# Kernel tuning notes

Measured on AMD Instinct MI355X. Metric: run time of the kernel, lower is better.

Reference implementation:

```python
import jax, jax.numpy as jnp
import numpy as np

N_CLASSES = 9
INPUT_SIZE = N_CLASSES + 1  # 10
HIDDEN = 512
BATCH = 256
SEQ = 1024


def setup_inputs() -> dict:
    key = jax.random.key(0)
    ks = jax.random.split(key, 7)
    s_ih = 1.0 / np.sqrt(HIDDEN)
    inputs = jax.random.normal(ks[0], (BATCH, SEQ, INPUT_SIZE), dtype=jnp.float32)
    # LSTMCell params (PyTorch layout: [4H, in], gate order i,f,g,o)
    W_ih = jax.random.uniform(ks[1], (4 * HIDDEN, INPUT_SIZE), jnp.float32, -s_ih, s_ih)
    W_hh = jax.random.uniform(ks[2], (4 * HIDDEN, HIDDEN), jnp.float32, -s_ih, s_ih)
    b_ih = jax.random.uniform(ks[3], (4 * HIDDEN,), jnp.float32, -s_ih, s_ih)
    b_hh = jax.random.uniform(ks[4], (4 * HIDDEN,), jnp.float32, -s_ih, s_ih)
    # Output projection: kaiming_normal_ (fan_in = HIDDEN, relu gain sqrt(2)), zero bias
    lin_W = jax.random.normal(ks[5], (N_CLASSES, HIDDEN), dtype=jnp.float32) * np.float32(np.sqrt(2.0 / HIDDEN))
    lin_b = jnp.zeros((N_CLASSES,), dtype=jnp.float32)
    return {"inputs": inputs, "W_ih": W_ih, "W_hh": W_hh, "b_ih": b_ih,
            "b_hh": b_hh, "lin_W": lin_W, "lin_b": lin_b}


def reference(inputs, W_ih, W_hh, b_ih, b_hh, lin_W, lin_b):
    B = inputs.shape[0]
    H = W_hh.shape[1]
    # Precompute input contributions for all steps in one big GEMM: [B,T,4H]
    x_gates = jnp.einsum('bti,gi->btg', inputs, W_ih) + b_ih + b_hh

    def step(carry, xg_t):
        h, c = carry
        gates = xg_t + h @ W_hh.T  # [B, 4H]
        i, f, g, o = jnp.split(gates, 4, axis=-1)
        i = jax.nn.sigmoid(i)
        f = jax.nn.sigmoid(f)
        g = jnp.tanh(g)
        o = jax.nn.sigmoid(o)
        c = f * c + i * g
        h = o * jnp.tanh(c)
        return (h, c), h

    h0 = jnp.zeros((B, H), dtype=inputs.dtype)
    c0 = jnp.zeros((B, H), dtype=inputs.dtype)
    _, hs = jax.lax.scan(step, (h0, c0), jnp.swapaxes(x_gates, 0, 1))  # hs: [T,B,H]
    # Per-step Linear, batched into one GEMM: [B,T,n_classes]
    logits = jnp.einsum('tbh,ch->btc', hs, lin_W) + lin_b
    return logits
```

## Files before the change

kernel.cpp:

```cpp
#include <hip/hip_runtime.h>

typedef unsigned int u32;
typedef unsigned long long u64;
typedef unsigned short u16;
typedef short bfrag __attribute__((ext_vector_type(8)));
typedef float f4 __attribute__((ext_vector_type(4)));
typedef u32 u32x4 __attribute__((ext_vector_type(4)));

#define HID 512
#define SEQT 1024
#define NIN 10
#define NC 9
#define NCL 16
#define MB  16
#define KSN 17
#define HROW 512
#define LROW 516

#define WPACK_U16 (16*4*2*KSN*64*8)
#define WPACK_BYTES (WPACK_U16*2)
#define HEX_U16 (NCL*2*MB*HROW)
#define HEX_BYTES (HEX_U16*2)
#define FLAGS_U32 (NCL*64)
#define FLAGS_BYTES (FLAGS_U32*4)

__device__ __forceinline__ u16 f2b(float f){
  u32 u = __float_as_uint(f);
  return (u16)((u + 0x7fffu + ((u>>16)&1u)) >> 16);
}
__device__ __forceinline__ float b2f(u16 b){ return __uint_as_float(((u32)b)<<16); }
__device__ __forceinline__ float sigm(float x){ return 1.f/(1.f+__expf(-x)); }
__device__ __forceinline__ float tanh_(float x){ float e=__expf(2.f*x); return 1.f - 2.f/(e+1.f); }

__device__ __forceinline__ void st32_sys(u64 base, u32 off, u32 v){
  asm volatile("global_store_dword %0, %1, %2 sc0 sc1" :: "v"(off), "v"(v), "s"(base) : "memory");
}
__device__ __forceinline__ void st128_sys(u64 base, u32 off, u32x4 v){
  asm volatile("global_store_dwordx4 %0, %1, %2 sc0 sc1" :: "v"(off), "v"(v), "s"(base) : "memory");
}
__device__ __forceinline__ void drain_vm(){
  asm volatile("s_waitcnt vmcnt(0)" ::: "memory");
}
__device__ __forceinline__ void spin_flags(u64 flgb, u32 foff, u32 tgt){
  u32 v0, v1 = 0;
  asm volatile("global_load_dword %0, %1, %2 sc0 sc1" : "=&v"(v0) : "v"(foff), "s"(flgb) : "memory");
  int guard = 0;
  for(;;){
    asm volatile("global_load_dword %0, %1, %2 sc0 sc1\n\ts_waitcnt vmcnt(1)"
                 : "=&v"(v1) : "v"(foff), "s"(flgb) : "memory");
    if (__all((int)(v0 >= tgt))) break;
    asm volatile("global_load_dword %0, %1, %2 sc0 sc1\n\ts_waitcnt vmcnt(1)"
                 : "=&v"(v0) : "v"(foff), "s"(flgb) : "memory");
    if (__all((int)(v1 >= tgt))) break;
    if ((guard += 2) > 400000) break;
  }
  drain_vm();
  asm volatile("" :: "v"(v0), "v"(v1));
}

__global__ void pack_kernel(const float* __restrict__ W_ih, const float* __restrict__ W_hh,
                            const float* __restrict__ b_ih, const float* __restrict__ b_hh,
                            u16* __restrict__ Wpack)
{
  int tid = blockIdx.x*256 + threadIdx.x;
  if (tid >= 16*4*2*KSN*64) return;
  int lane = tid & 63;
  int rest = tid >> 6;
  int ks = rest % KSN; rest /= KSN;
  int p = rest & 1; rest >>= 1;
  int w = rest & 3; rest >>= 2;
  int g = rest;
  int c2 = lane & 15;
  int kb = lane >> 4;
  int j = g*32 + w*8 + (c2 & 7);
  int gate = (p ? 2 : 0) + (c2 >= 8 ? 1 : 0);
  int R = gate*HID + j;

  union { u16 s[8]; bfrag v; } o;
  if (ks < 16) {
    const float* src = W_hh + (size_t)R*HID + ks*32 + kb*8;
    #pragma unroll
    for (int e=0;e<8;e++) o.s[e] = f2b(src[e]);
  } else {
    #pragma unroll
    for (int e=0;e<8;e++) {
      int k = kb*8 + e;
      float v = (k < NIN) ? W_ih[(size_t)R*NIN + k] : (k==NIN ? (b_ih[R]+b_hh[R]) : 0.f);
      o.s[e] = f2b(v);
    }
  }
  *(bfrag*)(Wpack + (size_t)tid*8) = o.v;
}

__global__ void init_kernel(u16* __restrict__ hex_, u32* __restrict__ flags)
{
  int tid = blockIdx.x*256 + threadIdx.x;
  if (tid < HEX_U16) hex_[tid] = 0;
  if (tid < FLAGS_U32) flags[tid] = 0;
}

__global__ __launch_bounds__(256, 1) void lstm_kernel(
    const float* __restrict__ inputs, const float* __restrict__ lin_W,
    const float* __restrict__ lin_b, const u16* __restrict__ Wpack,
    u16* __restrict__ hex_, u32* __restrict__ flags, float* __restrict__ out)
{
  const int bid = blockIdx.x;
  const int cl = bid >> 4;
  const int g = bid & 15;
  const int tid = threadIdx.x;
  const int w = tid >> 6;
  const int lane = tid & 63;
  const int c2 = lane & 15;
  const int kb = lane >> 4;
  const int jb = g*32 + w*8;
  const bool lowhalf = (c2 < 8);
  const int vb = cl*MB + g;

  __shared__ __align__(16) u16 panel[MB*LROW];
  __shared__ __align__(16) u16 rowbuf[2][HID];

  bfrag wf0[KSN], wf1[KSN];
  {
    const u16* base = Wpack + ((size_t)(g*4+w)*2)*KSN*64*8;
    #pragma unroll
    for (int ks=0;ks<KSN;ks++) wf0[ks] = *(const bfrag*)(base + ((size_t)ks*64 + lane)*8);
    #pragma unroll
    for (int ks=0;ks<KSN;ks++) wf1[ks] = *(const bfrag*)(base + ((size_t)(KSN+ks)*64 + lane)*8);
  }
  float lw[3][8]; float lb[3];
  if (w < 3) {
    #pragma unroll
    for (int cc=0;cc<3;cc++){
      int cls = w*3+cc;
      lb[cc] = lin_b[cls];
      #pragma unroll
      for (int e=0;e<8;e++) lw[cc][e] = lin_W[(size_t)cls*HID + lane*8 + e];
    }
  }

  float cst[4] = {0.f,0.f,0.f,0.f};

  const u64 ex0 = (u64)(hex_ + (size_t)(cl*2+0)*MB*HROW);
  const u64 ex1 = (u64)(hex_ + (size_t)(cl*2+1)*MB*HROW);
  const u64 flgb = (u64)(flags + (size_t)cl*64);
  const u32 foff = (u32)(lane*4);

  u32 go[4], lo[4];
  #pragma unroll
  for (int i=0;i<4;i++){
    u32 chunk = (u32)tid + (u32)i*256u;
    go[i] = (chunk>>6)*1024u + (chunk&63u)*16u;
    lo[i] = (chunk>>6)*(LROW*2u) + (chunk&63u)*16u;
  }

  const float* xrow = inputs + (size_t)(cl*MB + c2)*SEQT*NIN;

  for (int t = 0; t < SEQT; ++t) {
    const u64 cur = (t & 1) ? ex1 : ex0;
    const u64 nxt = (t & 1) ? ex0 : ex1;

    union { u32 u[4]; bfrag v; } xu;
    xu.u[0]=0; xu.u[1]=0; xu.u[2]=0; xu.u[3]=0;
    {
      const float* p = xrow + (size_t)t*NIN;
      if (kb == 0) {
        #pragma unroll
        for (int q=0;q<4;q++) xu.u[q] = (u32)f2b(p[2*q]) | ((u32)f2b(p[2*q+1])<<16);
      } else if (kb == 1) {
        xu.u[0] = (u32)f2b(p[8]) | ((u32)f2b(p[9])<<16);
        xu.u[1] = 0x3F80u;
      }
    }

    if (w == 0) spin_flags(flgb, foff, (u32)t);
    __syncthreads();

    u32x4 r0,r1,r2,r3;
    asm volatile(
      "global_load_dwordx4 %0, %4, %8 sc0 sc1\n\t"
      "global_load_dwordx4 %1, %5, %8 sc0 sc1\n\t"
      "global_load_dwordx4 %2, %6, %8 sc0 sc1\n\t"
      "global_load_dwordx4 %3, %7, %8 sc0 sc1"
      : "=&v"(r0), "=&v"(r1), "=&v"(r2), "=&v"(r3)
      : "v"(go[0]), "v"(go[1]), "v"(go[2]), "v"(go[3]), "s"(cur)
      : "memory");

    if (w < 3 && t >= 2) {
      bfrag hx = *(const bfrag*)&rowbuf[(t-1)&1][lane*8];
      float hv[8];
      #pragma unroll
      for (int e=0;e<8;e++) hv[e] = b2f((u16)hx[e]);
      #pragma unroll
      for (int cc=0;cc<3;cc++){
        float s = 0.f;
        #pragma unroll
        for (int e=0;e<8;e++) s += hv[e]*lw[cc][e];
        #pragma unroll
        for (int off=1;off<64;off<<=1) s += __shfl_xor(s, off, 64);
        if (lane == 0)
          out[((size_t)vb*SEQT + (t-2))*NC + (w*3+cc)] = s + lb[cc];
      }
    }

    drain_vm();
    __builtin_amdgcn_sched_barrier(0);
    *(u32x4*)((char*)panel + lo[0]) = r0;
    *(u32x4*)((char*)panel + lo[1]) = r1;
    *(u32x4*)((char*)panel + lo[2]) = r2;
    *(u32x4*)((char*)panel + lo[3]) = r3;
    __syncthreads();

    if (w == 3)
      *(bfrag*)&rowbuf[t&1][lane*8] = *(const bfrag*)&panel[g*LROW + lane*8];

    f4 acc0 = {0.f,0.f,0.f,0.f}, acc1 = {0.f,0.f,0.f,0.f};
    #pragma unroll
    for (int ks=0;ks<16;ks++){
      bfrag av = *(const bfrag*)&panel[c2*LROW + ks*32 + kb*8];
      acc0 = __builtin_amdgcn_mfma_f32_16x16x32_bf16(av, wf0[ks], acc0, 0,0,0);
      acc1 = __builtin_amdgcn_mfma_f32_16x16x32_bf16(av, wf1[ks], acc1, 0,0,0);
    }
    acc0 = __builtin_amdgcn_mfma_f32_16x16x32_bf16(xu.v, wf0[16], acc0, 0,0,0);
    acc1 = __builtin_amdgcn_mfma_f32_16x16x32_bf16(xu.v, wf1[16], acc1, 0,0,0);

    u16 hb[4];
    #pragma unroll
    for (int r=0;r<4;r++){
      float a0 = sigm(acc0[r]);
      float a1 = lowhalf ? tanh_(acc1[r]) : sigm(acc1[r]);
      float p0 = __shfl_xor(a0, 8, 64);
      float p1 = __shfl_xor(a1, 8, 64);
      float ii = lowhalf ? a0 : p0;
      float ff = lowhalf ? p0 : a0;
      float gg = lowhalf ? a1 : p1;
      float oo = lowhalf ? p1 : a1;
      float cn = ff*cst[r] + ii*gg;
      cst[r] = cn;
      hb[r] = f2b(oo * tanh_(cn));
    }

    #pragma unroll
    for (int r=0;r<4;r++){
      u32 pv = (u32)hb[r] | (((u32)(u16)__shfl_down((int)hb[r], 1, 64)) << 16);
      u32 p1 = __shfl_down(pv, 2, 64);
      u32 p2 = __shfl_down(pv, 4, 64);
      u32 p3 = __shfl_down(pv, 6, 64);
      if (c2 == 0) {
        u32x4 pk = {pv, p1, p2, p3};
        st128_sys(nxt, (u32)((kb*4+r)*1024 + jb*2), pk);
      }
    }

    drain_vm();
    if (lane == 0)
      st32_sys(flgb, (u32)((g*4+w)*4), (u32)(t+1));
  }

  if (w == 0) spin_flags(flgb, foff, (u32)SEQT);
  __syncthreads();
  if (w < 3) {
    {
      bfrag hx = *(const bfrag*)&rowbuf[(SEQT-1)&1][lane*8];
      float hv[8];
      #pragma unroll
      for (int e=0;e<8;e++) hv[e] = b2f((u16)hx[e]);
      #pragma unroll
      for (int cc=0;cc<3;cc++){
        float s = 0.f;
        #pragma unroll
        for (int e=0;e<8;e++) s += hv[e]*lw[cc][e];
        #pragma unroll
        for (int off=1;off<64;off<<=1) s += __shfl_xor(s, off, 64);
        if (lane == 0)
          out[((size_t)vb*SEQT + (SEQT-2))*NC + (w*3+cc)] = s + lb[cc];
      }
    }
    {
      u32x4 rr;
      asm volatile("global_load_dwordx4 %0, %1, %2 sc0 sc1\n\ts_waitcnt vmcnt(0)"
                   : "=&v"(rr) : "v"((u32)(g*1024 + lane*16)), "s"(ex0) : "memory");
      float hv[8];
      #pragma unroll
      for (int e=0;e<4;e++){
        hv[2*e]   = b2f((u16)(rr[e] & 0xffffu));
        hv[2*e+1] = b2f((u16)(rr[e] >> 16));
      }
      #pragma unroll
      for (int cc=0;cc<3;cc++){
        float s = 0.f;
        #pragma unroll
        for (int e=0;e<8;e++) s += hv[e]*lw[cc][e];
        #pragma unroll
        for (int off=1;off<64;off<<=1) s += __shfl_xor(s, off, 64);
        if (lane == 0)
          out[((size_t)vb*SEQT + (SEQT-1))*NC + (w*3+cc)] = s + lb[cc];
      }
    }
  }
}

extern "C" void kernel_launch(void* const* d_in, const int* in_sizes, int n_in,
                              void* d_out, int out_size, void* d_ws, size_t ws_size,
                              hipStream_t stream)
{
  const float* inputs = (const float*)d_in[0];
  const float* W_ih   = (const float*)d_in[1];
  const float* W_hh   = (const float*)d_in[2];
  const float* b_ih   = (const float*)d_in[3];
  const float* b_hh   = (const float*)d_in[4];
  const float* lin_W  = (const float*)d_in[5];
  const float* lin_b  = (const float*)d_in[6];

  u16* Wpack = (u16*)d_ws;
  u16* hex_  = (u16*)((char*)d_ws + WPACK_BYTES);
  u32* flags = (u32*)((char*)d_ws + WPACK_BYTES + HEX_BYTES);

  pack_kernel<<<(16*4*2*KSN*64 + 255)/256, 256, 0, stream>>>(W_ih, W_hh, b_ih, b_hh, Wpack);
  init_kernel<<<(HEX_U16 + 255)/256, 256, 0, stream>>>(hex_, flags);
  lstm_kernel<<<256, 256, 0, stream>>>(inputs, lin_W, lin_b, Wpack, hex_, flags, (float*)d_out);
}
```

Before: 4.223 ms.

## Replace flag-based barrier with per-word tagged hidden-state exchange polling

Each bf16 hidden value is now stored with the timestep tag in the low 16 bits of a 32-bit word. Consumers poll the data itself until every tag matches, instead of waiting on separate per-wave flags and then reloading the data. This removes the store-drain, flag-store, flag-spin and second-load round trip on every step. The block's own slice is written straight into a double-buffered LDS panel, and the output projection reads the panel directly. In exchange the exchange traffic doubles in size, and the polling loads are repeated for any chunks not yet ready.

Measured after the change: 5.087 ms. 1.2x slower.

```diff
diff --git a/kernel.cpp b/kernel.cpp
--- a/kernel.cpp
+++ b/kernel.cpp
@@ -6,6 +6,7 @@
 typedef short bfrag __attribute__((ext_vector_type(8)));
 typedef float f4 __attribute__((ext_vector_type(4)));
 typedef u32 u32x4 __attribute__((ext_vector_type(4)));
+typedef u32 u32x2 __attribute__((ext_vector_type(2)));
 
 #define HID 512
 #define SEQT 1024
@@ -14,15 +15,12 @@
 #define NCL 16
 #define MB  16
 #define KSN 17
-#define HROW 512
 #define LROW 516
 
 #define WPACK_U16 (16*4*2*KSN*64*8)
 #define WPACK_BYTES (WPACK_U16*2)
-#define HEX_U16 (NCL*2*MB*HROW)
-#define HEX_BYTES (HEX_U16*2)
-#define FLAGS_U32 (NCL*64)
-#define FLAGS_BYTES (FLAGS_U32*4)
+#define HEX_U32 (NCL*2*MB*HID)
+#define HEX_BYTES (HEX_U32*4)
 
 __device__ __forceinline__ u16 f2b(float f){
   u32 u = __float_as_uint(f);
@@ -34,28 +32,6 @@
 
 __device__ __forceinline__ void st32_sys(u64 base, u32 off, u32 v){
   asm volatile("global_store_dword %0, %1, %2 sc0 sc1" :: "v"(off), "v"(v), "s"(base) : "memory");
-}
-__device__ __forceinline__ void st128_sys(u64 base, u32 off, u32x4 v){
-  asm volatile("global_store_dwordx4 %0, %1, %2 sc0 sc1" :: "v"(off), "v"(v), "s"(base) : "memory");
-}
-__device__ __forceinline__ void drain_vm(){
-  asm volatile("s_waitcnt vmcnt(0)" ::: "memory");
-}
-__device__ __forceinline__ void spin_flags(u64 flgb, u32 foff, u32 tgt){
-  u32 v0, v1 = 0;
-  asm volatile("global_load_dword %0, %1, %2 sc0 sc1" : "=&v"(v0) : "v"(foff), "s"(flgb) : "memory");
-  int guard = 0;
-  for(;;){
-    asm volatile("global_load_dword %0, %1, %2 sc0 sc1\n\ts_waitcnt vmcnt(1)"
-                 : "=&v"(v1) : "v"(foff), "s"(flgb) : "memory");
-    if (__all((int)(v0 >= tgt))) break;
-    asm volatile("global_load_dword %0, %1, %2 sc0 sc1\n\ts_waitcnt vmcnt(1)"
-                 : "=&v"(v0) : "v"(foff), "s"(flgb) : "memory");
-    if (__all((int)(v1 >= tgt))) break;
-    if ((guard += 2) > 400000) break;
-  }
-  drain_vm();
-  asm volatile("" :: "v"(v0), "v"(v1));
 }
 
 __global__ void pack_kernel(const float* __restrict__ W_ih, const float* __restrict__ W_hh,
@@ -92,17 +68,27 @@
   *(bfrag*)(Wpack + (size_t)tid*8) = o.v;
 }
 
-__global__ void init_kernel(u16* __restrict__ hex_, u32* __restrict__ flags)
+__global__ void init_kernel(u32* __restrict__ hexw)
 {
   int tid = blockIdx.x*256 + threadIdx.x;
-  if (tid < HEX_U16) hex_[tid] = 0;
-  if (tid < FLAGS_U32) flags[tid] = 0;
-}
+  if (tid < HEX_U32) hexw[tid] = 0;
+}
+
+#define PISS(i, vi) \
+  if (pend & (1u<<(i))) { \
+    asm volatile("global_load_dwordx4 %0, %1, %2 sc0 sc1" \
+                 : "=&v"(vi) : "v"(gof[i]), "s"(cur) : "memory"); }
+#define PCHK(i, vi) \
+  if (pend & (1u<<(i))) { \
+    if ((((vi[0]^tg)|(vi[1]^tg)|(vi[2]^tg)|(vi[3]^tg)) & 0xffffu) == 0u) { \
+      u32x2 pk = { (vi[0]>>16) | (vi[1]&0xffff0000u), (vi[2]>>16) | (vi[3]&0xffff0000u) }; \
+      *(u32x2*)((char*)panb + lof[i]) = pk; \
+      pend &= ~(1u<<(i)); } }
 
 __global__ __launch_bounds__(256, 1) void lstm_kernel(
     const float* __restrict__ inputs, const float* __restrict__ lin_W,
     const float* __restrict__ lin_b, const u16* __restrict__ Wpack,
-    u16* __restrict__ hex_, u32* __restrict__ flags, float* __restrict__ out)
+    u32* __restrict__ hexw, float* __restrict__ out)
 {
   const int bid = blockIdx.x;
   const int cl = bid >> 4;
@@ -116,8 +102,7 @@
   const bool lowhalf = (c2 < 8);
   const int vb = cl*MB + g;
 
-  __shared__ __align__(16) u16 panel[MB*LROW];
-  __shared__ __align__(16) u16 rowbuf[2][HID];
+  __shared__ __align__(16) u16 panel[2][MB*LROW];
 
   bfrag wf0[KSN], wf1[KSN];
   {
@@ -140,24 +125,29 @@
 
   float cst[4] = {0.f,0.f,0.f,0.f};
 
-  const u64 ex0 = (u64)(hex_ + (size_t)(cl*2+0)*MB*HROW);
-  const u64 ex1 = (u64)(hex_ + (size_t)(cl*2+1)*MB*HROW);
-  const u64 flgb = (u64)(flags + (size_t)cl*64);
-  const u32 foff = (u32)(lane*4);
-
-  u32 go[4], lo[4];
+  const u64 ex0 = (u64)(hexw + (size_t)(cl*2+0)*MB*HID);
+  const u64 ex1 = (u64)(hexw + (size_t)(cl*2+1)*MB*HID);
+
+  u32 gof[8], lof[8], pend0 = 0;
   #pragma unroll
-  for (int i=0;i<4;i++){
-    u32 chunk = (u32)tid + (u32)i*256u;
-    go[i] = (chunk>>6)*1024u + (chunk&63u)*16u;
-    lo[i] = (chunk>>6)*(LROW*2u) + (chunk&63u)*16u;
-  }
+  for (int i=0;i<8;i++){
+    u32 c = (u32)tid + (u32)i*256u;
+    u32 row = c >> 7, rem = c & 127u;
+    gof[i] = row*2048u + rem*16u;
+    lof[i] = row*(LROW*2u) + rem*8u;
+    if ((int)(rem >> 3) != g) pend0 |= (1u<<i);
+  }
+
+  for (int i = tid; i < MB*LROW; i += 256) panel[0][i] = 0;
 
   const float* xrow = inputs + (size_t)(cl*MB + c2)*SEQT*NIN;
 
   for (int t = 0; t < SEQT; ++t) {
     const u64 cur = (t & 1) ? ex1 : ex0;
     const u64 nxt = (t & 1) ? ex0 : ex1;
+    const u32 tg  = (u32)t;
+    const u32 tgn = (u32)(t+1);
+    u16* panb = &panel[t&1][0];
 
     union { u32 u[4]; bfrag v; } xu;
     xu.u[0]=0; xu.u[1]=0; xu.u[2]=0; xu.u[3]=0;
@@ -172,51 +162,27 @@
       }
     }
 
-    if (w == 0) spin_flags(flgb, foff, (u32)t);
+    {
+      u32 pend = pend0;
+      u32x4 v0,v1,v2,v3,v4,v5,v6,v7;
+      for (int gq = 0; pend && gq < 20000; ++gq) {
+        PISS(0,v0) PISS(1,v1) PISS(2,v2) PISS(3,v3)
+        PISS(4,v4) PISS(5,v5) PISS(6,v6) PISS(7,v7)
+        asm volatile("s_waitcnt vmcnt(0)" ::: "memory");
+        __builtin_amdgcn_sched_barrier(0);
+        PCHK(0,v0) PCHK(1,v1) PCHK(2,v2) PCHK(3,v3)
+        PCHK(4,v4) PCHK(5,v5) PCHK(6,v6) PCHK(7,v7)
+      }
+    }
     __syncthreads();
 
-    u32x4 r0,r1,r2,r3;
-    asm volatile(
-      "global_load_dwordx4 %0, %4, %8 sc0 sc1\n\t"
-      "global_load_dwordx4 %1, %5, %8 sc0 sc1\n\t"
-      "global_load_dwordx4 %2, %6, %8 sc0 sc1\n\t"
-      "global_load_dwordx4 %3, %7, %8 sc0 sc1"
-      : "=&v"(r0), "=&v"(r1), "=&v"(r2), "=&v"(r3)
-      : "v"(go[0]), "v"(go[1]), "v"(go[2]), "v"(go[3]), "s"(cur)
-      : "memory");
-
-    if (w < 3 && t >= 2) {
-      bfrag hx = *(const bfrag*)&rowbuf[(t-1)&1][lane*8];
-      float hv[8];
-      #pragma unroll
-      for (int e=0;e<8;e++) hv[e] = b2f((u16)hx[e]);
-      #pragma unroll
-      for (int cc=0;cc<3;cc++){
-        float s = 0.f;
-        #pragma unroll
-        for (int e=0;e<8;e++) s += hv[e]*lw[cc][e];
-        #pragma unroll
-        for (int off=1;off<64;off<<=1) s += __shfl_xor(s, off, 64);
-        if (lane == 0)
-          out[((size_t)vb*SEQT + (t-2))*NC + (w*3+cc)] = s + lb[cc];
-      }
-    }
-
-    drain_vm();
-    __builtin_amdgcn_sched_barrier(0);
-    *(u32x4*)((char*)panel + lo[0]) = r0;
-    *(u32x4*)((char*)panel + lo[1]) = r1;
-    *(u32x4*)((char*)panel + lo[2]) = r2;
-    *(u32x4*)((char*)panel + lo[3]) = r3;
-    __syncthreads();
-
-    if (w == 3)
-      *(bfrag*)&rowbuf[t&1][lane*8] = *(const bfrag*)&panel[g*LROW + lane*8];
+    bfrag hx;
+    if (w < 3) hx = *(const bfrag*)&panb[g*LROW + lane*8];
 
     f4 acc0 = {0.f,0.f,0.f,0.f}, acc1 = {0.f,0.f,0.f,0.f};
     #pragma unroll
     for (int ks=0;ks<16;ks++){
-      bfrag av = *(const bfrag*)&panel[c2*LROW + ks*32 + kb*8];
+      bfrag av = *(const bfrag*)&panb[c2*LROW + ks*32 + kb*8];
       acc0 = __builtin_amdgcn_mfma_f32_16x16x32_bf16(av, wf0[ks], acc0, 0,0,0);
       acc1 = __builtin_amdgcn_mfma_f32_16x16x32_bf16(av, wf1[ks], acc1, 0,0,0);
     }
@@ -239,28 +205,20 @@
       hb[r] = f2b(oo * tanh_(cn));
     }
 
-    #pragma unroll
-    for (int r=0;r<4;r++){
-      u32 pv = (u32)hb[r] | (((u32)(u16)__shfl_down((int)hb[r], 1, 64)) << 16);
-      u32 p1 = __shfl_down(pv, 2, 64);
-      u32 p2 = __shfl_down(pv, 4, 64);
-      u32 p3 = __shfl_down(pv, 6, 64);
-      if (c2 == 0) {
-        u32x4 pk = {pv, p1, p2, p3};
-        st128_sys(nxt, (u32)((kb*4+r)*1024 + jb*2), pk);
-      }
-    }
-
-    drain_vm();
-    if (lane == 0)
-      st32_sys(flgb, (u32)((g*4+w)*4), (u32)(t+1));
-  }
-
-  if (w == 0) spin_flags(flgb, foff, (u32)SEQT);
-  __syncthreads();
-  if (w < 3) {
     {
-      bfrag hx = *(const bfrag*)&rowbuf[(SEQT-1)&1][lane*8];
+      int col = jb + (c2 & 7);
+      u32 rowa = (u32)(kb*4 + (lowhalf ? 0 : 2));
+      u16 slo = lowhalf ? hb[0] : hb[2];
+      u16 shi = lowhalf ? hb[1] : hb[3];
+      u32 cb4 = (u32)(col*4);
+      st32_sys(nxt, rowa*2048u + cb4,        ((u32)slo<<16) | tgn);
+      st32_sys(nxt, rowa*2048u + 2048u + cb4, ((u32)shi<<16) | tgn);
+      u16* pn = &panel[(t+1)&1][0];
+      pn[rowa*LROW + col]     = slo;
+      pn[(rowa+1)*LROW + col] = shi;
+    }
+
+    if (w < 3 && t > 0) {
       float hv[8];
       #pragma unroll
       for (int e=0;e<8;e++) hv[e] = b2f((u16)hx[e]);
@@ -272,29 +230,44 @@
         #pragma unroll
         for (int off=1;off<64;off<<=1) s += __shfl_xor(s, off, 64);
         if (lane == 0)
-          out[((size_t)vb*SEQT + (SEQT-2))*NC + (w*3+cc)] = s + lb[cc];
+          out[((size_t)vb*SEQT + (t-1))*NC + (w*3+cc)] = s + lb[cc];
       }
     }
-    {
-      u32x4 rr;
-      asm volatile("global_load_dwordx4 %0, %1, %2 sc0 sc1\n\ts_waitcnt vmcnt(0)"
-                   : "=&v"(rr) : "v"((u32)(g*1024 + lane*16)), "s"(ex0) : "memory");
-      float hv[8];
-      #pragma unroll
-      for (int e=0;e<4;e++){
-        hv[2*e]   = b2f((u16)(rr[e] & 0xffffu));
-        hv[2*e+1] = b2f((u16)(rr[e] >> 16));
-      }
-      #pragma unroll
-      for (int cc=0;cc<3;cc++){
-        float s = 0.f;
-        #pragma unroll
-        for (int e=0;e<8;e++) s += hv[e]*lw[cc][e];
-        #pragma unroll
-        for (int off=1;off<64;off<<=1) s += __shfl_xor(s, off, 64);
-        if (lane == 0)
-          out[((size_t)vb*SEQT + (SEQT-1))*NC + (w*3+cc)] = s + lb[cc];
-      }
+  }
+
+  if (w < 3) {
+    u32 ge0 = (u32)(g*2048 + (lane*2)*16);
+    u32 ge1 = ge0 + 16u;
+    u32x4 e0, e1;
+    u32 pend = 3u;
+    const u32 tg = (u32)SEQT;
+    for (int gq = 0; pend && gq < 20000; ++gq) {
+      if (pend & 1u)
+        asm volatile("global_load_dwordx4 %0, %1, %2 sc0 sc1"
+                     : "=&v"(e0) : "v"(ge0), "s"(ex0) : "memory");
+      if (pend & 2u)
+        asm volatile("global_load_dwordx4 %0, %1, %2 sc0 sc1"
+                     : "=&v"(e1) : "v"(ge1), "s"(ex0) : "memory");
+      asm volatile("s_waitcnt vmcnt(0)" ::: "memory");
+      __builtin_amdgcn_sched_barrier(0);
+      if ((pend & 1u) && ((((e0[0]^tg)|(e0[1]^tg)|(e0[2]^tg)|(e0[3]^tg)) & 0xffffu)==0u)) pend &= ~1u;
+      if ((pend & 2u) && ((((e1[0]^tg)|(e1[1]^tg)|(e1[2]^tg)|(e1[3]^tg)) & 0xffffu)==0u)) pend &= ~2u;
+    }
+    float hv[8];
+    #pragma unroll
+    for (int e=0;e<4;e++){
+      hv[e]   = __uint_as_float(e0[e] & 0xffff0000u);
+      hv[4+e] = __uint_as_float(e1[e] & 0xffff0000u);
+    }
+    #pragma unroll
+    for (int cc=0;cc<3;cc++){
+      float s = 0.f;
+      #pragma unroll
+      for (int e=0;e<8;e++) s += hv[e]*lw[cc][e];
+      #pragma unroll
+      for (int off=1;off<64;off<<=1) s += __shfl_xor(s, off, 64);
+      if (lane == 0)
+        out[((size_t)vb*SEQT + (SEQT-1))*NC + (w*3+cc)] = s + lb[cc];
     }
   }
 }
@@ -312,10 +285,9 @@
   const float* lin_b  = (const float*)d_in[6];
 
   u16* Wpack = (u16*)d_ws;
-  u16* hex_  = (u16*)((char*)d_ws + WPACK_BYTES);
-  u32* flags = (u32*)((char*)d_ws + WPACK_BYTES + HEX_BYTES);
+  u32* hexw  = (u32*)((char*)d_ws + WPACK_BYTES);
 
   pack_kernel<<<(16*4*2*KSN*64 + 255)/256, 256, 0, stream>>>(W_ih, W_hh, b_ih, b_hh, Wpack);
-  init_kernel<<<(HEX_U16 + 255)/256, 256, 0, stream>>>(hex_, flags);
-  lstm_kernel<<<256, 256, 0, stream>>>(inputs, lin_W, lin_b, Wpack, hex_, flags, (float*)d_out);
-}
+  init_kernel<<<(HEX_U32 + 255)/256, 256, 0, stream>>>(hexw);
+  lstm_kernel<<<256, 256, 0, stream>>>(inputs, lin_W, lin_b, Wpack, hexw, (float*)d_out);
+}
```

## Interleave two batch groups per block to overlap cross-block sync latency

Applied to the files above, without the earlier changes.

Each block now processes two independent 16-row batch groups in alternation, so one group's flag wait and exchange can overlap the other group's compute. The grid is halved to 128 blocks, and each block uses 16 per-block flags instead of per-wave flags, with a __syncthreads before the flag store. The h exchange layout becomes contiguous and uses 32-bit stores, and the output projection reads h directly from the panel. The cost is serialized per-group work inside each block and extra barriers; with only 8 clusters, latency may still dominate.

Result: slower. 9.623 ms (+127.9%).

```diff
diff --git a/kernel.cpp b/kernel.cpp
--- a/kernel.cpp
+++ b/kernel.cpp
@@ -11,17 +11,18 @@
 #define SEQT 1024
 #define NIN 10
 #define NC 9
-#define NCL 16
-#define MB  16
+#define NCLS 8
+#define NG 2
+#define MB 16
 #define KSN 17
-#define HROW 512
 #define LROW 516
 
 #define WPACK_U16 (16*4*2*KSN*64*8)
 #define WPACK_BYTES (WPACK_U16*2)
-#define HEX_U16 (NCL*2*MB*HROW)
+#define PANEL_BYTES (MB*HID*2)
+#define HEX_U16 (NCLS*NG*2*MB*HID)
 #define HEX_BYTES (HEX_U16*2)
-#define FLAGS_U32 (NCL*64)
+#define FLAGS_U32 (NCLS*NG*64)
 #define FLAGS_BYTES (FLAGS_U32*4)
 
 __device__ __forceinline__ u16 f2b(float f){
@@ -35,27 +36,18 @@
 __device__ __forceinline__ void st32_sys(u64 base, u32 off, u32 v){
   asm volatile("global_store_dword %0, %1, %2 sc0 sc1" :: "v"(off), "v"(v), "s"(base) : "memory");
 }
-__device__ __forceinline__ void st128_sys(u64 base, u32 off, u32x4 v){
-  asm volatile("global_store_dwordx4 %0, %1, %2 sc0 sc1" :: "v"(off), "v"(v), "s"(base) : "memory");
-}
 __device__ __forceinline__ void drain_vm(){
   asm volatile("s_waitcnt vmcnt(0)" ::: "memory");
 }
 __device__ __forceinline__ void spin_flags(u64 flgb, u32 foff, u32 tgt){
-  u32 v0, v1 = 0;
-  asm volatile("global_load_dword %0, %1, %2 sc0 sc1" : "=&v"(v0) : "v"(foff), "s"(flgb) : "memory");
   int guard = 0;
   for(;;){
-    asm volatile("global_load_dword %0, %1, %2 sc0 sc1\n\ts_waitcnt vmcnt(1)"
-                 : "=&v"(v1) : "v"(foff), "s"(flgb) : "memory");
-    if (__all((int)(v0 >= tgt))) break;
-    asm volatile("global_load_dword %0, %1, %2 sc0 sc1\n\ts_waitcnt vmcnt(1)"
-                 : "=&v"(v0) : "v"(foff), "s"(flgb) : "memory");
-    if (__all((int)(v1 >= tgt))) break;
-    if ((guard += 2) > 400000) break;
-  }
-  drain_vm();
-  asm volatile("" :: "v"(v0), "v"(v1));
+    u32 v;
+    asm volatile("global_load_dword %0, %1, %2 sc0 sc1\n\ts_waitcnt vmcnt(0)"
+                 : "=&v"(v) : "v"(foff), "s"(flgb) : "memory");
+    if (__all((int)(v >= tgt))) break;
+    if (++guard > 200000) break;
+  }
 }
 
 __global__ void pack_kernel(const float* __restrict__ W_ih, const float* __restrict__ W_hh,
@@ -114,10 +106,8 @@
   const int kb = lane >> 4;
   const int jb = g*32 + w*8;
   const bool lowhalf = (c2 < 8);
-  const int vb = cl*MB + g;
-
-  __shared__ __align__(16) u16 panel[MB*LROW];
-  __shared__ __align__(16) u16 rowbuf[2][HID];
+
+  __shared__ __align__(16) u16 panel[NG][MB*LROW];
 
   bfrag wf0[KSN], wf1[KSN];
   {
@@ -138,58 +128,143 @@
     }
   }
 
-  float cst[4] = {0.f,0.f,0.f,0.f};
-
-  const u64 ex0 = (u64)(hex_ + (size_t)(cl*2+0)*MB*HROW);
-  const u64 ex1 = (u64)(hex_ + (size_t)(cl*2+1)*MB*HROW);
-  const u64 flgb = (u64)(flags + (size_t)cl*64);
-  const u32 foff = (u32)(lane*4);
+  float cst[NG][4] = {{0.f,0.f,0.f,0.f},{0.f,0.f,0.f,0.f}};
+
+  u64 exp0[NG], exp1[NG], flgb[NG];
+  const float* xrow[NG];
+  int vb[NG];
+  #pragma unroll
+  for (int grp=0; grp<NG; ++grp){
+    exp0[grp] = (u64)((char*)hex_ + (size_t)((cl*NG+grp)*2+0)*PANEL_BYTES);
+    exp1[grp] = (u64)((char*)hex_ + (size_t)((cl*NG+grp)*2+1)*PANEL_BYTES);
+    flgb[grp] = (u64)(flags + (size_t)(cl*NG+grp)*64);
+    xrow[grp] = inputs + (size_t)(cl*32 + grp*16 + c2)*SEQT*NIN;
+    vb[grp]   = cl*32 + grp*16 + g;
+  }
+  const u32 foff = (u32)(c2*4);
 
   u32 go[4], lo[4];
   #pragma unroll
   for (int i=0;i<4;i++){
     u32 chunk = (u32)tid + (u32)i*256u;
-    go[i] = (chunk>>6)*1024u + (chunk&63u)*16u;
+    go[i] = chunk*16u;
     lo[i] = (chunk>>6)*(LROW*2u) + (chunk&63u)*16u;
   }
 
-  const float* xrow = inputs + (size_t)(cl*MB + c2)*SEQT*NIN;
-
   for (int t = 0; t < SEQT; ++t) {
-    const u64 cur = (t & 1) ? ex1 : ex0;
-    const u64 nxt = (t & 1) ? ex0 : ex1;
-
-    union { u32 u[4]; bfrag v; } xu;
-    xu.u[0]=0; xu.u[1]=0; xu.u[2]=0; xu.u[3]=0;
-    {
-      const float* p = xrow + (size_t)t*NIN;
-      if (kb == 0) {
+    #pragma unroll
+    for (int grp=0; grp<NG; ++grp) {
+      const u64 cur = (t & 1) ? exp1[grp] : exp0[grp];
+      const u64 nxt = (t & 1) ? exp0[grp] : exp1[grp];
+      u16* panb = &panel[grp][0];
+
+      spin_flags(flgb[grp], foff, (u32)t);
+
+      u32x4 r0,r1,r2,r3;
+      asm volatile(
+        "global_load_dwordx4 %0, %4, %8 sc0 sc1\n\t"
+        "global_load_dwordx4 %1, %5, %8 sc0 sc1\n\t"
+        "global_load_dwordx4 %2, %6, %8 sc0 sc1\n\t"
+        "global_load_dwordx4 %3, %7, %8 sc0 sc1"
+        : "=&v"(r0), "=&v"(r1), "=&v"(r2), "=&v"(r3)
+        : "v"(go[0]), "v"(go[1]), "v"(go[2]), "v"(go[3]), "s"(cur)
+        : "memory");
+
+      union { u32 u[4]; bfrag v; } xu;
+      xu.u[0]=0; xu.u[1]=0; xu.u[2]=0; xu.u[3]=0;
+      {
+        const float* p = xrow[grp] + (size_t)t*NIN;
+        if (kb == 0) {
+          #pragma unroll
+          for (int q=0;q<4;q++) xu.u[q] = (u32)f2b(p[2*q]) | ((u32)f2b(p[2*q+1])<<16);
+        } else if (kb == 1) {
+          xu.u[0] = (u32)f2b(p[8]) | ((u32)f2b(p[9])<<16);
+          xu.u[1] = 0x3F80u;
+        }
+      }
+
+      drain_vm();
+      __builtin_amdgcn_sched_barrier(0);
+      *(u32x4*)((char*)panb + lo[0]) = r0;
+      *(u32x4*)((char*)panb + lo[1]) = r1;
+      *(u32x4*)((char*)panb + lo[2]) = r2;
+      *(u32x4*)((char*)panb + lo[3]) = r3;
+      __syncthreads();
+
+      bfrag hx;
+      if (w < 3) hx = *(const bfrag*)&panb[g*LROW + lane*8];
+
+      f4 acc0 = {0.f,0.f,0.f,0.f}, acc1 = {0.f,0.f,0.f,0.f};
+      #pragma unroll
+      for (int ks=0;ks<16;ks++){
+        bfrag av = *(const bfrag*)&panb[c2*LROW + ks*32 + kb*8];
+        acc0 = __builtin_amdgcn_mfma_f32_16x16x32_bf16(av, wf0[ks], acc0, 0,0,0);
+        acc1 = __builtin_amdgcn_mfma_f32_16x16x32_bf16(av, wf1[ks], acc1, 0,0,0);
+      }
+      acc0 = __builtin_amdgcn_mfma_f32_16x16x32_bf16(xu.v, wf0[16], acc0, 0,0,0);
+      acc1 = __builtin_amdgcn_mfma_f32_16x16x32_bf16(xu.v, wf1[16], acc1, 0,0,0);
+
+      u16 hb[4];
+      #pragma unroll
+      for (int r=0;r<4;r++){
+        float a0 = sigm(acc0[r]);
+        float a1 = lowhalf ? tanh_(acc1[r]) : sigm(acc1[r]);
+        float p0 = __shfl_xor(a0, 8, 64);
+        float p1 = __shfl_xor(a1, 8, 64);
+        float ii = lowhalf ? a0 : p0;
+        float ff = lowhalf ? p0 : a0;
+        float gg = lowhalf ? a1 : p1;
+        float oo = lowhalf ? p1 : a1;
+        float cn = ff*cst[grp][r] + ii*gg;
+        cst[grp][r] = cn;
+        hb[r] = f2b(oo * tanh_(cn));
+      }
+
+      #pragma unroll
+      for (int r=0;r<4;r++){
+        u32 nb = (u32)(u16)__shfl_down((int)hb[r], 1, 64);
+        if (lowhalf && !(c2 & 1)) {
+          u32 pv = (u32)hb[r] | (nb << 16);
+          st32_sys(nxt, (u32)((kb*4+r)*1024 + (jb + c2)*2), pv);
+        }
+      }
+
+      drain_vm();
+      __syncthreads();
+      if (tid == 0)
+        st32_sys(flgb[grp], (u32)(g*4), (u32)(t+1));
+
+      if (w < 3 && t > 0) {
+        float hv[8];
         #pragma unroll
-        for (int q=0;q<4;q++) xu.u[q] = (u32)f2b(p[2*q]) | ((u32)f2b(p[2*q+1])<<16);
-      } else if (kb == 1) {
-        xu.u[0] = (u32)f2b(p[8]) | ((u32)f2b(p[9])<<16);
-        xu.u[1] = 0x3F80u;
+        for (int e=0;e<8;e++) hv[e] = b2f((u16)hx[e]);
+        #pragma unroll
+        for (int cc=0;cc<3;cc++){
+          float s = 0.f;
+          #pragma unroll
+          for (int e=0;e<8;e++) s += hv[e]*lw[cc][e];
+          #pragma unroll
+          for (int off=1;off<64;off<<=1) s += __shfl_xor(s, off, 64);
+          if (lane == 0)
+            out[((size_t)vb[grp]*SEQT + (t-1))*NC + (w*3+cc)] = s + lb[cc];
+        }
       }
     }
-
-    if (w == 0) spin_flags(flgb, foff, (u32)t);
-    __syncthreads();
-
-    u32x4 r0,r1,r2,r3;
-    asm volatile(
-      "global_load_dwordx4 %0, %4, %8 sc0 sc1\n\t"
-      "global_load_dwordx4 %1, %5, %8 sc0 sc1\n\t"
-      "global_load_dwordx4 %2, %6, %8 sc0 sc1\n\t"
-      "global_load_dwordx4 %3, %7, %8 sc0 sc1"
-      : "=&v"(r0), "=&v"(r1), "=&v"(r2), "=&v"(r3)
-      : "v"(go[0]), "v"(go[1]), "v"(go[2]), "v"(go[3]), "s"(cur)
-      : "memory");
-
-    if (w < 3 && t >= 2) {
-      bfrag hx = *(const bfrag*)&rowbuf[(t-1)&1][lane*8];
+  }
+
+  #pragma unroll
+  for (int grp=0; grp<NG; ++grp) {
+    spin_flags(flgb[grp], foff, (u32)SEQT);
+    if (w < 3) {
+      u32x4 rr;
+      asm volatile("global_load_dwordx4 %0, %1, %2 sc0 sc1\n\ts_waitcnt vmcnt(0)"
+                   : "=&v"(rr) : "v"((u32)(g*1024 + lane*16)), "s"(exp0[grp]) : "memory");
       float hv[8];
       #pragma unroll
-      for (int e=0;e<8;e++) hv[e] = b2f((u16)hx[e]);
+      for (int e=0;e<4;e++){
+        hv[2*e]   = b2f((u16)(rr[e] & 0xffffu));
+        hv[2*e+1] = b2f((u16)(rr[e] >> 16));
+      }
       #pragma unroll
       for (int cc=0;cc<3;cc++){
         float s = 0.f;
@@ -198,102 +273,7 @@
         #pragma unroll
         for (int off=1;off<64;off<<=1) s += __shfl_xor(s, off, 64);
         if (lane == 0)
-          out[((size_t)vb*SEQT + (t-2))*NC + (w*3+cc)] = s + lb[cc];
-      }
-    }
-
-    drain_vm();
-    __builtin_amdgcn_sched_barrier(0);
-    *(u32x4*)((char*)panel + lo[0]) = r0;
-    *(u32x4*)((char*)panel + lo[1]) = r1;
-    *(u32x4*)((char*)panel + lo[2]) = r2;
-    *(u32x4*)((char*)panel + lo[3]) = r3;
-    __syncthreads();
-
-    if (w == 3)
-      *(bfrag*)&rowbuf[t&1][lane*8] = *(const bfrag*)&panel[g*LROW + lane*8];
-
-    f4 acc0 = {0.f,0.f,0.f,0.f}, acc1 = {0.f,0.f,0.f,0.f};
-    #pragma unroll
-    for (int ks=0;ks<16;ks++){
-      bfrag av = *(const bfrag*)&panel[c2*LROW + ks*32 + kb*8];
-      acc0 = __builtin_amdgcn_mfma_f32_16x16x32_bf16(av, wf0[ks], acc0, 0,0,0);
-      acc1 = __builtin_amdgcn_mfma_f32_16x16x32_bf16(av, wf1[ks], acc1, 0,0,0);
-    }
-    acc0 = __builtin_amdgcn_mfma_f32_16x16x32_bf16(xu.v, wf0[16], acc0, 0,0,0);
-    acc1 = __builtin_amdgcn_mfma_f32_16x16x32_bf16(xu.v, wf1[16], acc1, 0,0,0);
-
-    u16 hb[4];
-    #pragma unroll
-    for (int r=0;r<4;r++){
-      float a0 = sigm(acc0[r]);
-      float a1 = lowhalf ? tanh_(acc1[r]) : sigm(acc1[r]);
-      float p0 = __shfl_xor(a0, 8, 64);
-      float p1 = __shfl_xor(a1, 8, 64);
-      float ii = lowhalf ? a0 : p0;
-      float ff = lowhalf ? p0 : a0;
-      float gg = lowhalf ? a1 : p1;
-      float oo = lowhalf ? p1 : a1;
-      float cn = ff*cst[r] + ii*gg;
-      cst[r] = cn;
-      hb[r] = f2b(oo * tanh_(cn));
-    }
-
-    #pragma unroll
-    for (int r=0;r<4;r++){
-      u32 pv = (u32)hb[r] | (((u32)(u16)__shfl_down((int)hb[r], 1, 64)) << 16);
-      u32 p1 = __shfl_down(pv, 2, 64);
-      u32 p2 = __shfl_down(pv, 4, 64);
-      u32 p3 = __shfl_down(pv, 6, 64);
-      if (c2 == 0) {
-        u32x4 pk = {pv, p1, p2, p3};
-        st128_sys(nxt, (u32)((kb*4+r)*1024 + jb*2), pk);
-      }
-    }
-
-    drain_vm();
-    if (lane == 0)
-      st32_sys(flgb, (u32)((g*4+w)*4), (u32)(t+1));
-  }
-
-  if (w == 0) spin_flags(flgb, foff, (u32)SEQT);
-  __syncthreads();
-  if (w < 3) {
-    {
-      bfrag hx = *(const bfrag*)&rowbuf[(SEQT-1)&1][lane*8];
-      float hv[8];
-      #pragma unroll
-      for (int e=0;e<8;e++) hv[e] = b2f((u16)hx[e]);
-      #pragma unroll
-      for (int cc=0;cc<3;cc++){
-        float s = 0.f;
-        #pragma unroll
-        for (int e=0;e<8;e++) s += hv[e]*lw[cc][e];
-        #pragma unroll
-        for (int off=1;off<64;off<<=1) s += __shfl_xor(s, off, 64);
-        if (lane == 0)
-          out[((size_t)vb*SEQT + (SEQT-2))*NC + (w*3+cc)] = s + lb[cc];
-      }
-    }
-    {
-      u32x4 rr;
-      asm volatile("global_load_dwordx4 %0, %1, %2 sc0 sc1\n\ts_waitcnt vmcnt(0)"
-                   : "=&v"(rr) : "v"((u32)(g*1024 + lane*16)), "s"(ex0) : "memory");
-      float hv[8];
-      #pragma unroll
-      for (int e=0;e<4;e++){
-        hv[2*e]   = b2f((u16)(rr[e] & 0xffffu));
-        hv[2*e+1] = b2f((u16)(rr[e] >> 16));
-      }
-      #pragma unroll
-      for (int cc=0;cc<3;cc++){
-        float s = 0.f;
-        #pragma unroll
-        for (int e=0;e<8;e++) s += hv[e]*lw[cc][e];
-        #pragma unroll
-        for (int off=1;off<64;off<<=1) s += __shfl_xor(s, off, 64);
-        if (lane == 0)
-          out[((size_t)vb*SEQT + (SEQT-1))*NC + (w*3+cc)] = s + lb[cc];
+          out[((size_t)vb[grp]*SEQT + (SEQT-1))*NC + (w*3+cc)] = s + lb[cc];
       }
     }
   }
@@ -317,5 +297,5 @@
 
   pack_kernel<<<(16*4*2*KSN*64 + 255)/256, 256, 0, stream>>>(W_ih, W_hh, b_ih, b_hh, Wpack);
   init_kernel<<<(HEX_U16 + 255)/256, 256, 0, stream>>>(hex_, flags);
-  lstm_kernel<<<256, 256, 0, stream>>>(inputs, lin_W, lin_b, Wpack, hex_, flags, (float*)d_out);
-}
+  lstm_kernel<<<128, 256, 0, stream>>>(inputs, lin_W, lin_b, Wpack, hex_, flags, (float*)d_out);
+}
```
